# Performance work log

Measured on AMD Instinct MI355X. Metric: run time of the kernel, lower is better.

## Reference

```python
import jax, jax.numpy as jnp
import numpy as np

N, D, C, K, M = 32768, 512, 64, 16, 128
DEPTH = 4            # log2(K): decision-tree depth per codebook
NODES = K - 1        # 15 internal tree nodes per codebook


def _build_selection_matrix():
    # Node i of the binary tree lives at level log2(i+1) and thresholds the
    # level-l selected dimension of its codebook.
    S = np.zeros((C * NODES, C * DEPTH), dtype=np.float32)
    base = np.zeros((NODES, DEPTH), dtype=np.float32)
    for i in range(NODES):
        base[i, int(np.log2(i + 1))] = 1.0
    for c in range(C):
        S[c * NODES:(c + 1) * NODES, c * DEPTH:(c + 1) * DEPTH] = base
    return S


def _build_bit_matrix():
    # Leaf k scores +1/-1 on each of its DEPTH ancestor nodes; the true leaf
    # attains the maximal score DEPTH.
    base = np.zeros((K, NODES), dtype=np.float32)
    for k in range(K):
        for l in range(DEPTH):
            node = (1 << l) - 1 + (k >> (DEPTH - l))   # ancestor at level l
            bit = (k >> (DEPTH - 1 - l)) & 1            # right(1)/left(0)
            base[k, node] = 1.0 if bit else -1.0
    B = np.zeros((C * K, C * NODES), dtype=np.float32)
    for c in range(C):
        B[c * K:(c + 1) * K, c * NODES:(c + 1) * NODES] = base
    return B


def setup_inputs() -> dict:
    key = jax.random.key(0)
    k1, k2, k3, k4 = jax.random.split(key, 4)
    I = jax.random.normal(k1, (N, D), jnp.float32)
    T = jax.random.normal(k2, (C * NODES,), jnp.float32) * 0.1   # thresholds
    L = jax.random.normal(k3, (M, C, K), jnp.float32)            # LUT
    dims = jnp.sort(jax.random.randint(k4, (C * DEPTH,), 0, D))  # selected cols
    S = jnp.asarray(_build_selection_matrix())
    B = jnp.asarray(_build_bit_matrix())
    temp = jnp.ones((1,), jnp.float32)
    return {"I": I, "T": T, "L": L, "S": S, "B": B, "dims": dims, "temp": temp}


def reference(I, T, L, S, B, dims, temp):
    t = temp[0]
    x_sel = I[:, dims]                                  # (N, C*DEPTH) gather
    h = x_sel @ S.T - T                                 # (N, C*NODES)
    tanh_h = jnp.tanh(h / t)
    # straight-through sign: forward sign(h), backward d(tanh(h/t))
    sign_ste = jnp.sign(h) - jax.lax.stop_gradient(tanh_h) + tanh_h
    b = sign_ste @ B.T                                  # (N, C*K) leaf scores
    soft = jax.nn.softmax(b.reshape(-1, C, K) / t, axis=2)
    hard = jax.nn.one_hot(jnp.argmax(soft, axis=2), K, dtype=soft.dtype)
    # straight-through one-hot encoding E: forward hard, backward soft
    E = hard - jax.lax.stop_gradient(soft) + soft       # (N, C, K)
    return jnp.einsum("nck,mck->nm", E, L)              # LUT gather-sum readout
```

## Files before the change

kernel.cpp:

```cpp
#include <hip/hip_runtime.h>

#define N_TOTAL 32768
#define D_DIM   512
#define C_DIM   64
#define K_DIM   16
#define M_DIM   128
#define NODES_  15

typedef unsigned short u16;
typedef unsigned int   u32;
typedef unsigned long long u64;
typedef unsigned char  u8;
typedef float  f32x4   __attribute__((ext_vector_type(4)));
typedef short  short8v __attribute__((ext_vector_type(8)));

#define WAIT_VM(N) asm volatile("s_waitcnt vmcnt(" #N ")" ::: "memory")

__device__ __forceinline__ u32 f2bf_bits(float f) {
    u32 u = __float_as_uint(f);
    return (u + 0x7FFFu + ((u >> 16) & 1u)) >> 16;
}

__device__ __forceinline__ void gload_lds16(const float* g, float* l) {
    __builtin_amdgcn_global_load_lds(
        (const __attribute__((address_space(1))) void*)g,
        (__attribute__((address_space(3))) void*)l, 16, 0, 0);
}

__global__ __launch_bounds__(256) void build_lbf(
    const float* __restrict__ L, u16* __restrict__ Lbf)
{
    int idx  = blockIdx.x * 256 + threadIdx.x;
    int lane = idx & 63;
    int ch   = (idx >> 6) & 31;
    int ct   = idx >> 11;
    int m  = ct * 16 + (lane & 15);
    int k0 = ch * 32 + ((lane >> 4) * 8);
    const float* src = L + (size_t)m * 1024 + k0;
    float4 a = *(const float4*)(src);
    float4 b = *(const float4*)(src + 4);
    u32 w0 = f2bf_bits(a.x) | (f2bf_bits(a.y) << 16);
    u32 w1 = f2bf_bits(a.z) | (f2bf_bits(a.w) << 16);
    u32 w2 = f2bf_bits(b.x) | (f2bf_bits(b.y) << 16);
    u32 w3 = f2bf_bits(b.z) | (f2bf_bits(b.w) << 16);
    *(uint4*)(Lbf + (size_t)idx * 8) = make_uint4(w0, w1, w2, w3);
}

__global__ __launch_bounds__(256) void mega_kernel(
    const float* __restrict__ I,
    const float* __restrict__ T,
    const int* __restrict__ dims,
    const u16* __restrict__ Lbf,
    float* __restrict__ out)
{
    __shared__ float sI[2 * 16 * D_DIM];
    __shared__ float sT[C_DIM * NODES_];
    __shared__ u8    sC2[C_DIM * 68];

    const int tid  = threadIdx.x;
    const int lane = tid & 63;
    const int wv   = tid >> 6;
    const int rowBase = blockIdx.x * 64;

    const int4 dml = ((const int4*)dims)[lane];

    auto issue = [&](int ci, int buf) {
        const float* src = I + (size_t)(rowBase + ci * 16 + wv * 4) * D_DIM;
        float* dst = sI + buf * 16 * D_DIM + wv * 4 * D_DIM;
        #pragma unroll
        for (int i = 0; i < 8; ++i)
            gload_lds16(src + i * 256 + lane * 4, dst + i * 256);
    };

    u32 c4[4] = {0u, 0u, 0u, 0u};
    const float* tc = sT + lane * NODES_;

    auto descend = [&](int buf, int ci) {
        #pragma unroll
        for (int rr = 0; rr < 4; ++rr) {
            const float* v = sI + buf * 16 * D_DIM + (wv * 4 + rr) * D_DIM;
            float x0 = v[dml.x], x1 = v[dml.y], x2 = v[dml.z], x3 = v[dml.w];
            int node = 0, k = 0;
            int b0 = (x0 - tc[0] > 0.0f) ? 1 : 0;
            k = b0; node = 1 + b0;
            int b1 = (x1 - tc[node] > 0.0f) ? 1 : 0;
            k = (k << 1) | b1; node = (node << 1) + 1 + b1;
            int b2 = (x2 - tc[node] > 0.0f) ? 1 : 0;
            k = (k << 1) | b2; node = (node << 1) + 1 + b2;
            int b3 = (x3 - tc[node] > 0.0f) ? 1 : 0;
            k = (k << 1) | b3;
            c4[rr] |= (u32)k << (8 * ci);
        }
    };

    issue(0, 0);
    for (int j = tid; j < C_DIM * NODES_; j += 256) sT[j] = T[j];
    __syncthreads();
    issue(1, 1);

    descend(0, 0);
    issue(2, 0);
    WAIT_VM(8);
    descend(1, 1);
    issue(3, 1);
    WAIT_VM(8);
    descend(0, 2);
    WAIT_VM(0);
    descend(1, 3);

    #pragma unroll
    for (int rr = 0; rr < 4; ++rr)
        *(u32*)(sC2 + lane * 68 + (wv * 4 + rr) * 4) = c4[rr];
    __syncthreads();

    const int l15     = lane & 15;
    const int clsLane = (lane >> 5) & 1;
    const int kb      = ((lane >> 4) & 1) * 8;

    f32x4 acc[4][2] = {};

    const u16* lb0 = Lbf + ((size_t)(wv * 2 + 0) * 32 * 64 + lane) * 8;
    const u16* lb1 = Lbf + ((size_t)(wv * 2 + 1) * 32 * 64 + lane) * 8;

    #pragma unroll 4
    for (int ch = 0; ch < 32; ++ch) {
        union { uint4 u; short8v v; } b0, b1;
        b0.u = *(const uint4*)(lb0 + (size_t)ch * 64 * 8);
        b1.u = *(const uint4*)(lb1 + (size_t)ch * 64 * 8);
        const int cls = ch * 2 + clsLane;
        const u32 codes4 = *(const u32*)(sC2 + cls * 68 + l15 * 4);
        #pragma unroll
        for (int rt = 0; rt < 4; ++rt) {
            u32 cd = (codes4 >> (8 * rt)) & 0xFFu;
            u32 tt = cd - (u32)kb;
            u64 sv = 0x3F80ull << ((tt & 3) * 16);
            union { u64 d[2]; short8v v; } a;
            a.d[0] = (tt < 4) ? sv : 0ull;
            a.d[1] = (tt >= 4 && tt < 8) ? sv : 0ull;
            acc[rt][0] = __builtin_amdgcn_mfma_f32_16x16x32_bf16(
                             a.v, b0.v, acc[rt][0], 0, 0, 0);
            acc[rt][1] = __builtin_amdgcn_mfma_f32_16x16x32_bf16(
                             a.v, b1.v, acc[rt][1], 0, 0, 0);
        }
    }

    #pragma unroll
    for (int rt = 0; rt < 4; ++rt) {
        #pragma unroll
        for (int cj = 0; cj < 2; ++cj) {
            int col = (wv * 2 + cj) * 16 + l15;
            int r0  = rowBase + rt * 16 + ((lane >> 4) << 2);
            float* o = out + (size_t)r0 * M_DIM + col;
            o[0 * M_DIM] = acc[rt][cj][0];
            o[1 * M_DIM] = acc[rt][cj][1];
            o[2 * M_DIM] = acc[rt][cj][2];
            o[3 * M_DIM] = acc[rt][cj][3];
        }
    }
}

extern "C" void kernel_launch(void* const* d_in, const int* in_sizes, int n_in,
                              void* d_out, int out_size, void* d_ws, size_t ws_size,
                              hipStream_t stream) {
    const float* I    = (const float*)d_in[0];
    const float* T    = (const float*)d_in[1];
    const float* L    = (const float*)d_in[2];
    const int*   dims = (const int*)d_in[5];

    u16* Lbf = (u16*)d_ws;

    hipLaunchKernelGGL(build_lbf, dim3(64), dim3(256), 0, stream, L, Lbf);
    hipLaunchKernelGGL(mega_kernel, dim3(N_TOTAL / 64), dim3(256), 0, stream,
                       I, T, dims, Lbf, (float*)d_out);
}
```

Baseline: 117.7 us.

## Split row block into halves and overlap second-half loads with first GEMM

Each block's 64 input rows are now loaded as eight 8-row chunks through a 4-slot LDS ring with deeper prefetch. Tree descent runs on the first 32 rows, and the MFMA readout for them starts while the loads for the last 32 rows are still in flight. The second half is then descended and its GEMM pass runs, hiding global-load latency behind matrix work. Launch bounds now request 2 blocks per CU, and code packing into LDS is rearranged to fit the half-split layout. This adds an extra barrier, and the tighter register budget may cause spills.

```diff
diff --git a/kernel.cpp b/kernel.cpp
--- a/kernel.cpp
+++ b/kernel.cpp
@@ -6,6 +6,7 @@
 #define K_DIM   16
 #define M_DIM   128
 #define NODES_  15
+#define ROWS_B  64
 
 typedef unsigned short u16;
 typedef unsigned int   u32;
@@ -19,6 +20,12 @@
 __device__ __forceinline__ u32 f2bf_bits(float f) {
     u32 u = __float_as_uint(f);
     return (u + 0x7FFFu + ((u >> 16) & 1u)) >> 16;
+}
+
+__device__ __forceinline__ void lds_barrier() {
+    asm volatile("s_waitcnt lgkmcnt(0)" ::: "memory");
+    __builtin_amdgcn_s_barrier();
+    asm volatile("" ::: "memory");
 }
 
 __device__ __forceinline__ void gload_lds16(const float* g, float* l) {
@@ -46,39 +53,39 @@
     *(uint4*)(Lbf + (size_t)idx * 8) = make_uint4(w0, w1, w2, w3);
 }
 
-__global__ __launch_bounds__(256) void mega_kernel(
+__global__ __launch_bounds__(256, 2) void mega_kernel(
     const float* __restrict__ I,
     const float* __restrict__ T,
     const int* __restrict__ dims,
     const u16* __restrict__ Lbf,
     float* __restrict__ out)
 {
-    __shared__ float sI[2 * 16 * D_DIM];
+    __shared__ float sI[4 * 8 * D_DIM];
     __shared__ float sT[C_DIM * NODES_];
     __shared__ u8    sC2[C_DIM * 68];
 
     const int tid  = threadIdx.x;
     const int lane = tid & 63;
     const int wv   = tid >> 6;
-    const int rowBase = blockIdx.x * 64;
+    const int rowBase = blockIdx.x * ROWS_B;
 
     const int4 dml = ((const int4*)dims)[lane];
 
-    auto issue = [&](int ci, int buf) {
-        const float* src = I + (size_t)(rowBase + ci * 16 + wv * 4) * D_DIM;
-        float* dst = sI + buf * 16 * D_DIM + wv * 4 * D_DIM;
+    auto issue = [&](int ci) {
+        const float* src = I + (size_t)(rowBase + ci * 8 + wv * 2) * D_DIM;
+        float* dst = sI + (ci & 3) * 8 * D_DIM + wv * 2 * D_DIM;
         #pragma unroll
-        for (int i = 0; i < 8; ++i)
+        for (int i = 0; i < 4; ++i)
             gload_lds16(src + i * 256 + lane * 4, dst + i * 256);
     };
 
-    u32 c4[4] = {0u, 0u, 0u, 0u};
+    u32 lo[2] = {0u, 0u}, hi[2] = {0u, 0u};
     const float* tc = sT + lane * NODES_;
 
-    auto descend = [&](int buf, int ci) {
+    auto descend = [&](int ci, u32* c2, int sh) {
         #pragma unroll
-        for (int rr = 0; rr < 4; ++rr) {
-            const float* v = sI + buf * 16 * D_DIM + (wv * 4 + rr) * D_DIM;
+        for (int rr = 0; rr < 2; ++rr) {
+            const float* v = sI + (ci & 3) * 8 * D_DIM + (wv * 2 + rr) * D_DIM;
             float x0 = v[dml.x], x1 = v[dml.y], x2 = v[dml.z], x3 = v[dml.w];
             int node = 0, k = 0;
             int b0 = (x0 - tc[0] > 0.0f) ? 1 : 0;
@@ -89,72 +96,98 @@
             k = (k << 1) | b2; node = (node << 1) + 1 + b2;
             int b3 = (x3 - tc[node] > 0.0f) ? 1 : 0;
             k = (k << 1) | b3;
-            c4[rr] |= (u32)k << (8 * ci);
+            c2[rr] |= (u32)k << sh;
         }
     };
 
-    issue(0, 0);
+    issue(0);
     for (int j = tid; j < C_DIM * NODES_; j += 256) sT[j] = T[j];
     __syncthreads();
-    issue(1, 1);
-
-    descend(0, 0);
-    issue(2, 0);
+
+    issue(1); issue(2);
+    descend(0, lo, 0);  issue(3);
     WAIT_VM(8);
-    descend(1, 1);
-    issue(3, 1);
+    descend(1, lo, 8);  issue(4);
     WAIT_VM(8);
-    descend(0, 2);
-    WAIT_VM(0);
-    descend(1, 3);
+    descend(2, lo, 16); issue(5);
+    WAIT_VM(8);
+    descend(3, lo, 24); issue(6); issue(7);
 
     #pragma unroll
-    for (int rr = 0; rr < 4; ++rr)
-        *(u32*)(sC2 + lane * 68 + (wv * 4 + rr) * 4) = c4[rr];
-    __syncthreads();
+    for (int rr = 0; rr < 2; ++rr) {
+        u32 w = lo[rr];
+        *(u16*)(sC2 + lane * 68 + (wv * 2 + rr) * 4) =
+            (u16)((w & 0xFFu) | ((w >> 8) & 0xFF00u));
+        *(u16*)(sC2 + lane * 68 + (8 + wv * 2 + rr) * 4) =
+            (u16)(((w >> 8) & 0xFFu) | ((w >> 16) & 0xFF00u));
+    }
+    lds_barrier();
 
     const int l15     = lane & 15;
     const int clsLane = (lane >> 5) & 1;
     const int kb      = ((lane >> 4) & 1) * 8;
 
-    f32x4 acc[4][2] = {};
-
     const u16* lb0 = Lbf + ((size_t)(wv * 2 + 0) * 32 * 64 + lane) * 8;
     const u16* lb1 = Lbf + ((size_t)(wv * 2 + 1) * 32 * 64 + lane) * 8;
 
-    #pragma unroll 4
-    for (int ch = 0; ch < 32; ++ch) {
-        union { uint4 u; short8v v; } b0, b1;
-        b0.u = *(const uint4*)(lb0 + (size_t)ch * 64 * 8);
-        b1.u = *(const uint4*)(lb1 + (size_t)ch * 64 * 8);
-        const int cls = ch * 2 + clsLane;
-        const u32 codes4 = *(const u32*)(sC2 + cls * 68 + l15 * 4);
-        #pragma unroll
-        for (int rt = 0; rt < 4; ++rt) {
-            u32 cd = (codes4 >> (8 * rt)) & 0xFFu;
-            u32 tt = cd - (u32)kb;
-            u64 sv = 0x3F80ull << ((tt & 3) * 16);
-            union { u64 d[2]; short8v v; } a;
-            a.d[0] = (tt < 4) ? sv : 0ull;
-            a.d[1] = (tt >= 4 && tt < 8) ? sv : 0ull;
-            acc[rt][0] = __builtin_amdgcn_mfma_f32_16x16x32_bf16(
-                             a.v, b0.v, acc[rt][0], 0, 0, 0);
-            acc[rt][1] = __builtin_amdgcn_mfma_f32_16x16x32_bf16(
-                             a.v, b1.v, acc[rt][1], 0, 0, 0);
+    f32x4 accA[2][2] = {};
+    f32x4 accB[2][2] = {};
+
+    auto gemm_pass = [&](f32x4 (&acc)[2][2], int rtsh) {
+        #pragma unroll 4
+        for (int ch = 0; ch < 32; ++ch) {
+            union { uint4 u; short8v v; } b0, b1;
+            b0.u = *(const uint4*)(lb0 + (size_t)ch * 64 * 8);
+            b1.u = *(const uint4*)(lb1 + (size_t)ch * 64 * 8);
+            const int cls = ch * 2 + clsLane;
+            const u32 codes4 = *(const u32*)(sC2 + cls * 68 + l15 * 4);
+            #pragma unroll
+            for (int rt = 0; rt < 2; ++rt) {
+                u32 cd = (codes4 >> (8 * (rt + rtsh))) & 0xFFu;
+                u32 tt = cd - (u32)kb;
+                u64 sv = 0x3F80ull << ((tt & 3) * 16);
+                union { u64 d[2]; short8v v; } a;
+                a.d[0] = (tt < 4) ? sv : 0ull;
+                a.d[1] = (tt >= 4 && tt < 8) ? sv : 0ull;
+                acc[rt][0] = __builtin_amdgcn_mfma_f32_16x16x32_bf16(
+                                 a.v, b0.v, acc[rt][0], 0, 0, 0);
+                acc[rt][1] = __builtin_amdgcn_mfma_f32_16x16x32_bf16(
+                                 a.v, b1.v, acc[rt][1], 0, 0, 0);
+            }
         }
+    };
+
+    gemm_pass(accA, 0);
+
+    WAIT_VM(0);
+    descend(4, hi, 0);
+    descend(5, hi, 8);
+    descend(6, hi, 16);
+    descend(7, hi, 24);
+    #pragma unroll
+    for (int rr = 0; rr < 2; ++rr) {
+        u32 w = hi[rr];
+        *(u16*)(sC2 + lane * 68 + (wv * 2 + rr) * 4 + 2) =
+            (u16)((w & 0xFFu) | ((w >> 8) & 0xFF00u));
+        *(u16*)(sC2 + lane * 68 + (8 + wv * 2 + rr) * 4 + 2) =
+            (u16)(((w >> 8) & 0xFFu) | ((w >> 16) & 0xFF00u));
     }
+    lds_barrier();
+
+    gemm_pass(accB, 2);
 
     #pragma unroll
     for (int rt = 0; rt < 4; ++rt) {
         #pragma unroll
         for (int cj = 0; cj < 2; ++cj) {
+            const f32x4 av = (rt < 2) ? accA[rt][cj] : accB[rt - 2][cj];
             int col = (wv * 2 + cj) * 16 + l15;
             int r0  = rowBase + rt * 16 + ((lane >> 4) << 2);
             float* o = out + (size_t)r0 * M_DIM + col;
-            o[0 * M_DIM] = acc[rt][cj][0];
-            o[1 * M_DIM] = acc[rt][cj][1];
-            o[2 * M_DIM] = acc[rt][cj][2];
-            o[3 * M_DIM] = acc[rt][cj][3];
+            o[0 * M_DIM] = av[0];
+            o[1 * M_DIM] = av[1];
+            o[2 * M_DIM] = av[2];
+            o[3 * M_DIM] = av[3];
         }
     }
 }
@@ -170,6 +203,6 @@
     u16* Lbf = (u16*)d_ws;
 
     hipLaunchKernelGGL(build_lbf, dim3(64), dim3(256), 0, stream, L, Lbf);
-    hipLaunchKernelGGL(mega_kernel, dim3(N_TOTAL / 64), dim3(256), 0, stream,
+    hipLaunchKernelGGL(mega_kernel, dim3(N_TOTAL / ROWS_B), dim3(256), 0, stream,
                        I, T, dims, Lbf, (float*)d_out);
 }
```

After: 118.5 us. About the same (+0.7%).
